# Performance work log

Hardware: AMD Instinct MI355X
Metric: run time of the kernel (lower is better)

Reference implementation:

```python
import jax, jax.numpy as jnp
import numpy as np

NCONF, NATOMS, NCOEFF = 64, 256, 45
NAOV = 12  # 4 p-vectors + 8 d-vectors (3 'diagonal' + 5 'off-diagonal' rows)

# hyperparameters (floats from the forward signature, fixed here)
LOW_S, UP_S = 0.5, 3.5
LOW_R, UP_R = 0.5, 3.5
LOW_A, UP_A = 0.5, 3.5
LOW_Z, UP_Z = 0.19634954, 2.94524311  # ~pi/16 .. 15*pi/16
OETA_S, OETA_R, OETA_A, OZETA = 16.0, 16.0, 8.0, 32.0


def setup_inputs() -> dict:
    key = jax.random.key(0)
    coefficients = jax.random.normal(key, (NCONF, NATOMS, NCOEFF), dtype=jnp.float32)
    return {"coefficients": coefficients, "NOShfS": 16, "NOShfR": 16, "NOShfA": 8, "NOShfZ": 8}


def _orbital_matrix(coefficients):
    n, a, _ = coefficients.shape
    p = coefficients[:, :, 9:21].reshape(n, a, 4, 3)
    d = coefficients[:, :, 21:45].reshape(n, a, 4, 6)
    d = d[..., jnp.array([0, 2, 5, 4, 3, 1])].reshape(n, a, 8, 3)
    # cat([p, d[:, :, :3], d[:, :, 3:]]) == cat([p, d])
    return jnp.concatenate([p, d], axis=2)  # [n, a, 12, 3]


def reference(coefficients, NOShfS, NOShfR, NOShfA, NOShfZ):
    # basis_functions='spd', use_simple_orbital_aev=False, use_angular_info=True
    n, a, _ = coefficients.shape
    om = _orbital_matrix(coefficients)                 # [n, a, 12, 3]
    dist = jnp.linalg.norm(om, axis=-1)                # [n, a, 12]

    shfS = jnp.linspace(LOW_S, UP_S, NOShfS)
    shfR = jnp.linspace(LOW_R, UP_R, NOShfR)
    s_aev = jnp.exp(-OETA_S * (dist[..., None] - shfS) ** 2)   # [n, a, 12, S]
    r_aev = jnp.exp(-OETA_R * (dist[..., None] - shfR) ** 2)   # [n, a, 12, R]
    radial = jnp.concatenate([s_aev, r_aev], axis=-1).reshape(n, a, NAOV * (NOShfS + NOShfR))

    # angles between all AOV pairs (vectorized version of the nested i<j loop)
    zero_mask = jnp.all(jnp.abs(om) < 1e-12, axis=-1)          # [n, a, 12]
    safe_d = jnp.where(zero_mask, 1.0, dist)
    nv = jnp.where(zero_mask[..., None], 0.0, om / safe_d[..., None])  # normalized AOVs
    iu, ju = np.triu_indices(NAOV, k=1)                        # 66 pairs, i-major order
    cos_ang = jnp.einsum('napk,napk->nap', nv[:, :, iu], nv[:, :, ju])  # [n, a, 66]
    angles = jnp.arccos(0.95 * cos_ang)
    avdist = 0.5 * (dist[:, :, iu] + dist[:, :, ju])           # [n, a, 66]

    shfZ = jnp.linspace(LOW_Z, UP_Z, NOShfZ)
    shfA = jnp.linspace(LOW_A, UP_A, NOShfA)
    factor1 = ((1.0 + jnp.cos(angles[..., None] - shfZ)) * 0.5) ** OZETA      # [n, a, 66, Z]
    factor2 = jnp.exp(-OETA_A * (avdist[..., None] - shfA) ** 2)              # [n, a, 66, A]
    angular = 2.0 * factor1[..., :, None] * factor2[..., None, :]             # [n, a, 66, Z, A]
    angular = angular.reshape(n, a, angles.shape[2] * NOShfZ * NOShfA)

    return jnp.concatenate([radial, angular], axis=-1)  # [n, a, 12*(S+R) + 66*Z*A]
```

## Files before the change

### kernel.cpp

```cpp
#include <hip/hip_runtime.h>
#include <math.h>

#define NCONF  64
#define NATOMS 256
#define NCOEFF 45
#define NAOV   12
#define NPAIR  66
#define RAD    384
#define ANG    4224
#define TOT    4608
#define APB    8

__constant__ unsigned char c_iu[NPAIR] = {
    0,0,0,0,0,0,0,0,0,0,0,
    1,1,1,1,1,1,1,1,1,1,
    2,2,2,2,2,2,2,2,2,
    3,3,3,3,3,3,3,3,
    4,4,4,4,4,4,4,
    5,5,5,5,5,5,
    6,6,6,6,6,
    7,7,7,7,
    8,8,8,
    9,9,
    10
};
__constant__ unsigned char c_ju[NPAIR] = {
    1,2,3,4,5,6,7,8,9,10,11,
    2,3,4,5,6,7,8,9,10,11,
    3,4,5,6,7,8,9,10,11,
    4,5,6,7,8,9,10,11,
    5,6,7,8,9,10,11,
    6,7,8,9,10,11,
    7,8,9,10,11,
    8,9,10,11,
    9,10,11,
    10,11,
    11
};

__constant__ float c_shfS[16] = {
    0.5f, 0.7f, 0.9f, 1.1f, 1.3f, 1.5f, 1.7f, 1.9f,
    2.1f, 2.3f, 2.5f, 2.7f, 2.9f, 3.1f, 3.3f, 3.5f
};
__constant__ float c_shfA[8] = {
    0.5f, 0.92857142857f, 1.35714285714f, 1.78571428571f,
    2.21428571429f, 2.64285714286f, 3.07142857143f, 3.5f
};
__constant__ float c_cosZ[8] = {
     0.98078528f,  0.83146961f,  0.55557023f,  0.19509032f,
    -0.19509032f, -0.55557023f, -0.83146961f, -0.98078528f
};
__constant__ float c_sinZ[8] = {
    0.19509032f, 0.55557023f, 0.83146961f, 0.98078528f,
    0.98078528f, 0.83146961f, 0.55557023f, 0.19509032f
};

__global__ __launch_bounds__(256, 8)
void OrbitalAEVComputer_40492951667225_kernel(const float* __restrict__ coef,
                                              float* __restrict__ out) {
    const int t = threadIdx.x;

    __shared__ float s_dist[2][NAOV];
    __shared__ float s_nv[2][NAOV][3];
    __shared__ float s_rad[2][NAOV * 16];
    __shared__ float s_f1[2][NPAIR * 8];
    __shared__ float s_f2[2][NPAIR * 8];

    const int atom0 = blockIdx.x * APB;

    for (int a = 0; a < APB; ++a) {
        const int buf = a & 1;
        const int atom = atom0 + a;
        const float* c = coef + (size_t)atom * NCOEFF;

        if (t < NAOV) {
            float x, y, z;
            if (t < 4) {
                x = c[9 + 3 * t]; y = c[10 + 3 * t]; z = c[11 + 3 * t];
            } else {
                int r = (t - 4) >> 1, h = (t - 4) & 1;
                const float* b = c + 21 + 6 * r;
                if (h == 0) { x = b[0]; y = b[2]; z = b[5]; }
                else        { x = b[4]; y = b[3]; z = b[1]; }
            }
            float d = sqrtf(x * x + y * y + z * z);
            bool zm = (fabsf(x) < 1e-12f) && (fabsf(y) < 1e-12f) && (fabsf(z) < 1e-12f);
            float inv = zm ? 0.0f : 1.0f / d;
            s_dist[buf][t] = d;
            s_nv[buf][t][0] = x * inv;
            s_nv[buf][t][1] = y * inv;
            s_nv[buf][t][2] = z * inv;
        }
        __syncthreads();

        for (int idx = t; idx < 1248; idx += 256) {
            if (idx < 192) {
                int p = idx >> 4, k = idx & 15;
                float dd = s_dist[buf][p] - c_shfS[k];
                s_rad[buf][idx] = __expf(-16.0f * dd * dd);
            } else if (idx < 720) {
                int jj = idx - 192;
                int q = jj >> 3, k = jj & 7;
                int i1 = c_iu[q], j1 = c_ju[q];
                float cang = s_nv[buf][i1][0] * s_nv[buf][j1][0]
                           + s_nv[buf][i1][1] * s_nv[buf][j1][1]
                           + s_nv[buf][i1][2] * s_nv[buf][j1][2];
                float c95 = 0.95f * cang;
                float sn  = sqrtf(fmaxf(1.0f - c95 * c95, 0.0f));
                float cosa = fmaf(c95, c_cosZ[k], sn * c_sinZ[k]);
                float x = 0.5f * (1.0f + cosa);
                x = x * x; x = x * x; x = x * x; x = x * x; x = x * x;
                s_f1[buf][jj] = x;
            } else {
                int jj = idx - 720;
                int q = jj >> 3, k = jj & 7;
                int i1 = c_iu[q], j1 = c_ju[q];
                float avd = 0.5f * (s_dist[buf][i1] + s_dist[buf][j1]);
                float dd = avd - c_shfA[k];
                s_f2[buf][jj] = __expf(-8.0f * dd * dd);
            }
        }
        __syncthreads();

        float* o = out + (size_t)atom * TOT;
        for (int idx4 = t; idx4 < TOT / 4; idx4 += 256) {
            float4 v;
            if (idx4 < 96) {
                int e = idx4 * 4;
                int p = e >> 5;
                int k0 = e & 31;
                const float* src = &s_rad[buf][p * 16 + (k0 & 15)];
                v = *reinterpret_cast<const float4*>(src);
            } else {
                int e = (idx4 - 96) * 4;
                int q = e >> 6;
                int z = (e >> 3) & 7;
                int a0 = e & 7;
                float f1v = 2.0f * s_f1[buf][q * 8 + z];
                const float4 f2v = *reinterpret_cast<const float4*>(&s_f2[buf][q * 8 + a0]);
                v.x = f1v * f2v.x;
                v.y = f1v * f2v.y;
                v.z = f1v * f2v.z;
                v.w = f1v * f2v.w;
            }
            reinterpret_cast<float4*>(o)[idx4] = v;
        }
    }
}

extern "C" void kernel_launch(void* const* d_in, const int* in_sizes, int n_in,
                              void* d_out, int out_size, void* d_ws, size_t ws_size,
                              hipStream_t stream) {
    const float* coef = (const float*)d_in[0];
    float* out = (float*)d_out;
    OrbitalAEVComputer_40492951667225_kernel<<<dim3(NCONF * NATOMS / APB), dim3(256), 0, stream>>>(coef, out);
}
```

Before: 320.6 us.

## Map one wavefront per atom, computing AEV features in registers without LDS

Each 64-lane wavefront now handles one atom. Every lane loads and normalizes all 12 orbital vectors into registers, and the block-wide shared-memory staging and __syncthreads barriers are gone. Each lane computes its own angular feature for all 66 pairs directly and writes it with nontemporal scalar stores, so the f1/f2 tables are no longer built in LDS. Work per output element goes up (transcendentals are recomputed per element instead of reused from a table, and stores are scalar instead of float4), in exchange for removing the barriers and the LDS traffic in this store-bound kernel.

```diff
diff --git a/kernel.cpp b/kernel.cpp
--- a/kernel.cpp
+++ b/kernel.cpp
@@ -9,34 +9,6 @@
 #define RAD    384
 #define ANG    4224
 #define TOT    4608
-#define APB    8
-
-__constant__ unsigned char c_iu[NPAIR] = {
-    0,0,0,0,0,0,0,0,0,0,0,
-    1,1,1,1,1,1,1,1,1,1,
-    2,2,2,2,2,2,2,2,2,
-    3,3,3,3,3,3,3,3,
-    4,4,4,4,4,4,4,
-    5,5,5,5,5,5,
-    6,6,6,6,6,
-    7,7,7,7,
-    8,8,8,
-    9,9,
-    10
-};
-__constant__ unsigned char c_ju[NPAIR] = {
-    1,2,3,4,5,6,7,8,9,10,11,
-    2,3,4,5,6,7,8,9,10,11,
-    3,4,5,6,7,8,9,10,11,
-    4,5,6,7,8,9,10,11,
-    5,6,7,8,9,10,11,
-    6,7,8,9,10,11,
-    7,8,9,10,11,
-    8,9,10,11,
-    9,10,11,
-    10,11,
-    11
-};
 
 __constant__ float c_shfS[16] = {
     0.5f, 0.7f, 0.9f, 1.1f, 1.3f, 1.5f, 1.7f, 1.9f,
@@ -55,95 +27,62 @@
     0.98078528f, 0.83146961f, 0.55557023f, 0.19509032f
 };
 
-__global__ __launch_bounds__(256, 8)
+__global__ __launch_bounds__(256, 4)
 void OrbitalAEVComputer_40492951667225_kernel(const float* __restrict__ coef,
                                               float* __restrict__ out) {
-    const int t = threadIdx.x;
+    const int lane = threadIdx.x & 63;
+    int atom = (int)(blockIdx.x * 4 + (threadIdx.x >> 6));
+    atom = __builtin_amdgcn_readfirstlane(atom);
+    const float* c = coef + (size_t)atom * NCOEFF;
 
-    __shared__ float s_dist[2][NAOV];
-    __shared__ float s_nv[2][NAOV][3];
-    __shared__ float s_rad[2][NAOV * 16];
-    __shared__ float s_f1[2][NPAIR * 8];
-    __shared__ float s_f2[2][NPAIR * 8];
+    float dist[NAOV], nx[NAOV], ny[NAOV], nz[NAOV];
+#pragma unroll
+    for (int p = 0; p < NAOV; ++p) {
+        float x, y, z;
+        if (p < 4) {
+            x = c[9 + 3 * p]; y = c[10 + 3 * p]; z = c[11 + 3 * p];
+        } else {
+            const int r = (p - 4) >> 1, h = (p - 4) & 1;
+            const float* b = c + 21 + 6 * r;
+            if (h == 0) { x = b[0]; y = b[2]; z = b[5]; }
+            else        { x = b[4]; y = b[3]; z = b[1]; }
+        }
+        const float d = sqrtf(x * x + y * y + z * z);
+        const bool zm = (fabsf(x) < 1e-12f) && (fabsf(y) < 1e-12f) && (fabsf(z) < 1e-12f);
+        const float inv = zm ? 0.0f : 1.0f / d;
+        dist[p] = d; nx[p] = x * inv; ny[p] = y * inv; nz[p] = z * inv;
+    }
 
-    const int atom0 = blockIdx.x * APB;
+    float* o = out + (size_t)atom * TOT;
 
-    for (int a = 0; a < APB; ++a) {
-        const int buf = a & 1;
-        const int atom = atom0 + a;
-        const float* c = coef + (size_t)atom * NCOEFF;
+    const float shf = c_shfS[lane & 15];
+#pragma unroll
+    for (int ch = 0; ch < 6; ++ch) {
+        const float d = (lane & 32) ? dist[2 * ch + 1] : dist[2 * ch];
+        const float dd = d - shf;
+        __builtin_nontemporal_store(__expf(-16.0f * dd * dd), o + ch * 64 + lane);
+    }
 
-        if (t < NAOV) {
-            float x, y, z;
-            if (t < 4) {
-                x = c[9 + 3 * t]; y = c[10 + 3 * t]; z = c[11 + 3 * t];
-            } else {
-                int r = (t - 4) >> 1, h = (t - 4) & 1;
-                const float* b = c + 21 + 6 * r;
-                if (h == 0) { x = b[0]; y = b[2]; z = b[5]; }
-                else        { x = b[4]; y = b[3]; z = b[1]; }
-            }
-            float d = sqrtf(x * x + y * y + z * z);
-            bool zm = (fabsf(x) < 1e-12f) && (fabsf(y) < 1e-12f) && (fabsf(z) < 1e-12f);
-            float inv = zm ? 0.0f : 1.0f / d;
-            s_dist[buf][t] = d;
-            s_nv[buf][t][0] = x * inv;
-            s_nv[buf][t][1] = y * inv;
-            s_nv[buf][t][2] = z * inv;
-        }
-        __syncthreads();
+    const float cz = c_cosZ[lane >> 3];
+    const float sz = c_sinZ[lane >> 3];
+    const float sa = c_shfA[lane & 7];
+    float* oa = o + RAD + lane;
 
-        for (int idx = t; idx < 1248; idx += 256) {
-            if (idx < 192) {
-                int p = idx >> 4, k = idx & 15;
-                float dd = s_dist[buf][p] - c_shfS[k];
-                s_rad[buf][idx] = __expf(-16.0f * dd * dd);
-            } else if (idx < 720) {
-                int jj = idx - 192;
-                int q = jj >> 3, k = jj & 7;
-                int i1 = c_iu[q], j1 = c_ju[q];
-                float cang = s_nv[buf][i1][0] * s_nv[buf][j1][0]
-                           + s_nv[buf][i1][1] * s_nv[buf][j1][1]
-                           + s_nv[buf][i1][2] * s_nv[buf][j1][2];
-                float c95 = 0.95f * cang;
-                float sn  = sqrtf(fmaxf(1.0f - c95 * c95, 0.0f));
-                float cosa = fmaf(c95, c_cosZ[k], sn * c_sinZ[k]);
-                float x = 0.5f * (1.0f + cosa);
-                x = x * x; x = x * x; x = x * x; x = x * x; x = x * x;
-                s_f1[buf][jj] = x;
-            } else {
-                int jj = idx - 720;
-                int q = jj >> 3, k = jj & 7;
-                int i1 = c_iu[q], j1 = c_ju[q];
-                float avd = 0.5f * (s_dist[buf][i1] + s_dist[buf][j1]);
-                float dd = avd - c_shfA[k];
-                s_f2[buf][jj] = __expf(-8.0f * dd * dd);
-            }
-        }
-        __syncthreads();
-
-        float* o = out + (size_t)atom * TOT;
-        for (int idx4 = t; idx4 < TOT / 4; idx4 += 256) {
-            float4 v;
-            if (idx4 < 96) {
-                int e = idx4 * 4;
-                int p = e >> 5;
-                int k0 = e & 31;
-                const float* src = &s_rad[buf][p * 16 + (k0 & 15)];
-                v = *reinterpret_cast<const float4*>(src);
-            } else {
-                int e = (idx4 - 96) * 4;
-                int q = e >> 6;
-                int z = (e >> 3) & 7;
-                int a0 = e & 7;
-                float f1v = 2.0f * s_f1[buf][q * 8 + z];
-                const float4 f2v = *reinterpret_cast<const float4*>(&s_f2[buf][q * 8 + a0]);
-                v.x = f1v * f2v.x;
-                v.y = f1v * f2v.y;
-                v.z = f1v * f2v.z;
-                v.w = f1v * f2v.w;
-            }
-            reinterpret_cast<float4*>(o)[idx4] = v;
+    int q = 0;
+#pragma unroll
+    for (int i = 0; i < NAOV - 1; ++i) {
+#pragma unroll
+        for (int j = i + 1; j < NAOV; ++j) {
+            const float cang = nx[i] * nx[j] + ny[i] * ny[j] + nz[i] * nz[j];
+            const float c95 = 0.95f * cang;
+            const float sn  = sqrtf(fmaxf(1.0f - c95 * c95, 0.0f));
+            const float cosa = fmaf(c95, cz, sn * sz);
+            float x = 0.5f + 0.5f * cosa;
+            x = x * x; x = x * x; x = x * x; x = x * x; x = x * x;
+            const float dd = 0.5f * (dist[i] + dist[j]) - sa;
+            const float f2 = __expf(-8.0f * dd * dd);
+            __builtin_nontemporal_store(2.0f * x * f2, oa + q * 64);
+            ++q;
         }
     }
 }
@@ -153,5 +92,5 @@
                               hipStream_t stream) {
     const float* coef = (const float*)d_in[0];
     float* out = (float*)d_out;
-    OrbitalAEVComputer_40492951667225_kernel<<<dim3(NCONF * NATOMS / APB), dim3(256), 0, stream>>>(coef, out);
+    OrbitalAEVComputer_40492951667225_kernel<<<dim3(NCONF * NATOMS / 4), dim3(256), 0, stream>>>(coef, out);
 }
```

Result: slower. 330.5 us (+3.1%).
